# Optimization experiments

Measured on AMD Instinct MI355X. Metric: run time of the kernel, lower is better.

Reference implementation:

```python
import jax, jax.numpy as jnp
import numpy as np
import math

B, S, D = 1, 2048, 2048
H, HD, KV = 16, 128, 1
E, F, TOPK = 8, 4096, 2
EPS = 1e-5


def setup_inputs() -> dict:
    key = jax.random.key(0)
    ks = jax.random.split(key, 14)
    sc = 0.02
    inp = {
        "x": jax.random.normal(ks[0], (B, S, D), dtype=jnp.float32),
        "wq": jax.random.normal(ks[1], (D, H * HD), dtype=jnp.float32) * sc,
        "wk": jax.random.normal(ks[2], (D, KV * HD), dtype=jnp.float32) * sc,
        "wv": jax.random.normal(ks[3], (D, KV * HD), dtype=jnp.float32) * sc,
        "wo": jax.random.normal(ks[4], (H * HD, D), dtype=jnp.float32) * sc,
        "w_router": jax.random.normal(ks[5], (D, E), dtype=jnp.float32) * sc,
        "w1": jax.random.normal(ks[6], (E, D, F), dtype=jnp.float32) * sc,
        "w3": jax.random.normal(ks[7], (E, D, F), dtype=jnp.float32) * sc,
        "w2": jax.random.normal(ks[8], (E, F, D), dtype=jnp.float32) * sc,
        "s_pre_mqa": jnp.ones((D,), dtype=jnp.float32),
        "s_post_mqa": jnp.ones((D,), dtype=jnp.float32),
        "s_pre_moe": jnp.ones((D,), dtype=jnp.float32),
        "s_post_moe": jnp.ones((D,), dtype=jnp.float32),
    }
    return inp


def _rmsnorm(x, scale):
    ms = jnp.mean(x * x, axis=-1, keepdims=True)
    return x * jax.lax.rsqrt(ms + EPS) * scale


def _mqa(h, wq, wk, wv, wo):
    b, s, _ = h.shape
    q = (h @ wq).reshape(b, s, H, HD)
    k = (h @ wk).reshape(b, s, KV, HD)
    v = (h @ wv).reshape(b, s, KV, HD)
    # repeat_interleave kv heads up to H (MQA)
    k = jnp.repeat(k, H // KV, axis=2)
    v = jnp.repeat(v, H // KV, axis=2)
    scale = 1.0 / math.sqrt(HD)
    scores = jnp.einsum("bqhd,bkhd->bhqk", q, k) * scale  # [B,H,S,S]
    causal = jnp.tril(jnp.ones((s, s), dtype=bool))
    scores = jnp.where(causal, scores, jnp.float32(-jnp.inf))
    attn = jax.nn.softmax(scores, axis=-1)
    out = jnp.einsum("bhqk,bkhd->bqhd", attn, v).reshape(b, s, H * HD)
    return out @ wo


def _moe(h, w_router, w1, w2, w3):
    logits = h @ w_router                        # [B,S,E]
    probs = jax.nn.softmax(logits, axis=-1)
    topv, topi = jax.lax.top_k(probs, TOPK)      # [B,S,K]
    topv = topv / jnp.sum(topv, axis=-1, keepdims=True)
    # combine weights per expert: [B,S,E]
    combine = jnp.sum(jax.nn.one_hot(topi, E, dtype=h.dtype) * topv[..., None], axis=-2)
    out = jnp.zeros_like(h)
    for e in range(E):  # fixed small expert count
        ye = (jax.nn.silu(h @ w1[e]) * (h @ w3[e])) @ w2[e]
        out = out + combine[..., e:e + 1] * ye
    return out, combine


def reference(x, wq, wk, wv, wo, w_router, w1, w2, w3,
              s_pre_mqa, s_post_mqa, s_pre_moe, s_post_moe):
    mqa_out = _mqa(_rmsnorm(x, s_pre_mqa), wq, wk, wv, wo)
    x = x + _rmsnorm(mqa_out, s_post_mqa)  # dropout p=0 (eval)
    moe_out, router_mask = _moe(_rmsnorm(x, s_pre_moe), w_router, w1, w2, w3)
    x = x + _rmsnorm(moe_out, s_post_moe)
    return x, router_mask
```

## Files before the change

kernel.cpp:

```cpp
#include <hip/hip_runtime.h>

#define S_LEN 2048
#define DM 2048
#define NHEAD 16
#define HDIM 128
#define NEXP 8
#define FF 4096
#define EPSV 1e-5f

typedef unsigned short u16;
typedef short bf16x8 __attribute__((ext_vector_type(8)));
typedef float f32x4 __attribute__((ext_vector_type(4)));

__device__ __forceinline__ f32x4 mfma16(bf16x8 a, bf16x8 b, f32x4 c) {
  return __builtin_amdgcn_mfma_f32_16x16x32_bf16(a, b, c, 0, 0, 0);
}

__device__ __forceinline__ float bf2f(u16 u) {
  union { unsigned int i; float f; } v; v.i = ((unsigned int)u) << 16; return v.f;
}
__device__ __forceinline__ u16 f2bf(float f) {
  union { float f; unsigned int i; } v; v.f = f;
  unsigned int u = v.i;
  return (u16)((u + 0x7fffu + ((u >> 16) & 1u)) >> 16);
}

__device__ __forceinline__ void gload_lds16(const u16* g, u16* l) {
  __builtin_amdgcn_global_load_lds(
      (const __attribute__((address_space(1))) unsigned int*)(unsigned long long)g,
      (__attribute__((address_space(3))) unsigned int*)(unsigned long long)l, 16, 0, 0);
}

__device__ __forceinline__ float blocksum(float v, float* sh) {
#pragma unroll
  for (int off = 32; off; off >>= 1) v += __shfl_xor(v, off, 64);
  const int w = threadIdx.x >> 6;
  if ((threadIdx.x & 63) == 0) sh[w] = v;
  __syncthreads();
  v = sh[0] + sh[1] + sh[2] + sh[3];
  __syncthreads();
  return v;
}

__device__ __forceinline__ void convsplit_body(char* lds, const float* __restrict__ src,
                                               int ld, u16* __restrict__ dhi,
                                               u16* __restrict__ dlo, int nblk, int kblk) {
  float(*tile)[65] = reinterpret_cast<float(*)[65]>(lds);
  const int n0 = nblk * 64, k0 = kblk * 64;
  const int t = threadIdx.x;
  {
    int r = t >> 4, c4 = (t & 15) * 4;
#pragma unroll
    for (int i = 0; i < 4; ++i) {
      float4 v = *reinterpret_cast<const float4*>(src + (size_t)(k0 + r + i * 16) * ld + n0 + c4);
      tile[r + i * 16][c4 + 0] = v.x;
      tile[r + i * 16][c4 + 1] = v.y;
      tile[r + i * 16][c4 + 2] = v.z;
      tile[r + i * 16][c4 + 3] = v.w;
    }
  }
  __syncthreads();
#pragma unroll
  for (int i = 0; i < 2; ++i) {
    int idx = i * 256 + t;
    int n = idx >> 3, kc = (idx & 7) * 8;
    bf16x8 hi, lo;
#pragma unroll
    for (int j = 0; j < 8; ++j) {
      float f = tile[kc + j][n];
      u16 hv = f2bf(f);
      hi[j] = (short)hv;
      lo[j] = (short)f2bf(f - bf2f(hv));
    }
    size_t o = (size_t)(n0 + n) * 2048 + k0 + kc;
    *reinterpret_cast<bf16x8*>(dhi + o) = hi;
    *reinterpret_cast<bf16x8*>(dlo + o) = lo;
  }
}

__global__ __launch_bounds__(256) void convsplit_kernel(
    const float* __restrict__ src, int ld, u16* __restrict__ dhi, u16* __restrict__ dlo) {
  __shared__ alignas(16) char lds[16640];
  convsplit_body(lds, src, ld, dhi, dlo, blockIdx.x, blockIdx.y);
}

__device__ __forceinline__ void convT_body(char* lds, const float* __restrict__ src,
                                           int R, int C, u16* __restrict__ dst,
                                           int nblk, int rblk, int e) {
  float(*tile)[65] = reinterpret_cast<float(*)[65]>(lds);
  const int n0 = nblk * 64, r0 = rblk * 64;
  const size_t bofs = (size_t)e * R * C;
  const int t = threadIdx.x;
  {
    int r = t >> 4, c4 = (t & 15) * 4;
#pragma unroll
    for (int i = 0; i < 4; ++i) {
      float4 v = *reinterpret_cast<const float4*>(src + bofs + (size_t)(r0 + r + i * 16) * C + n0 + c4);
      tile[r + i * 16][c4 + 0] = v.x;
      tile[r + i * 16][c4 + 1] = v.y;
      tile[r + i * 16][c4 + 2] = v.z;
      tile[r + i * 16][c4 + 3] = v.w;
    }
  }
  __syncthreads();
#pragma unroll
  for (int i = 0; i < 2; ++i) {
    int idx = i * 256 + t;
    int n = idx >> 3, kc = (idx & 7) * 8;
    bf16x8 pk;
#pragma unroll
    for (int j = 0; j < 8; ++j) pk[j] = (short)f2bf(tile[kc + j][n]);
    *reinterpret_cast<bf16x8*>(dst + bofs + (size_t)(n0 + n) * R + r0 + kc) = pk;
  }
}

__global__ __launch_bounds__(256) void rms_pre_kernel(
    const float* __restrict__ x, const float* __restrict__ s, u16* __restrict__ h1) {
  __shared__ float sh[4];
  const int row = blockIdx.x, t = threadIdx.x;
  const float* xr = x + (size_t)row * DM + t * 8;
  float4 a = *reinterpret_cast<const float4*>(xr);
  float4 b = *reinterpret_cast<const float4*>(xr + 4);
  float v[8] = {a.x, a.y, a.z, a.w, b.x, b.y, b.z, b.w};
  float ss = 0.f;
#pragma unroll
  for (int j = 0; j < 8; ++j) ss += v[j] * v[j];
  float inv = rsqrtf(blocksum(ss, sh) * (1.f / DM) + EPSV);
  const float* sp = s + t * 8;
  bf16x8 hi, lo;
#pragma unroll
  for (int j = 0; j < 8; ++j) {
    float val = v[j] * inv * sp[j];
    u16 hv = f2bf(val);
    hi[j] = (short)hv;
    lo[j] = (short)f2bf(val - bf2f(hv));
  }
  *reinterpret_cast<bf16x8*>(h1 + (size_t)row * 4096 + t * 8) = hi;
  *reinterpret_cast<bf16x8*>(h1 + (size_t)row * 4096 + 2048 + t * 8) = lo;
}

__device__ __forceinline__ void gemm3_body(
    char* lds, const u16* __restrict__ A, const u16* __restrict__ Bthi,
    const u16* __restrict__ Btlo, void* __restrict__ out,
    int mblk, int nblk, int mode, int ldc, int lo_off) {
  const int m0 = mblk * 128, n0 = nblk * 64;
  const int t = threadIdx.x, lane = t & 63, w = t >> 6;
  const int wm = (w >> 1) * 64, wn = (w & 1) * 32;
  const int l15 = lane & 15, lg = lane >> 4;
  const int wbase = t & ~63;

  u16* Ah = (u16*)lds;
  u16* Al = (u16*)(lds + 16384);
  u16* Bh = (u16*)(lds + 32768);
  u16* Bl = (u16*)(lds + 40960);

  const u16* Abh = A + (size_t)m0 * 4096;
  const u16* Abl = Abh + 2048;
  const u16* Bbh = Bthi + (size_t)n0 * 2048;
  const u16* Bbl = Btlo + (size_t)n0 * 2048;

  f32x4 acc[4][2];
#pragma unroll
  for (int m = 0; m < 4; ++m)
#pragma unroll
    for (int n = 0; n < 2; ++n) acc[m][n] = (f32x4){0.f, 0.f, 0.f, 0.f};

  for (int k0 = 0; k0 < 2048; k0 += 64) {
    __syncthreads();
#pragma unroll
    for (int i = 0; i < 4; ++i) {
      int p = i * 256 + t;
      int row = p >> 3;
      int csrc = (p & 7) ^ (row & 7);
      gload_lds16(Abh + (size_t)row * 4096 + k0 + csrc * 8, Ah + (i * 256 + wbase) * 8);
      gload_lds16(Abl + (size_t)row * 4096 + k0 + csrc * 8, Al + (i * 256 + wbase) * 8);
    }
#pragma unroll
    for (int i = 0; i < 2; ++i) {
      int p = i * 256 + t;
      int row = p >> 3;
      int csrc = (p & 7) ^ (row & 7);
      gload_lds16(Bbh + (size_t)row * 2048 + k0 + csrc * 8, Bh + (i * 256 + wbase) * 8);
      gload_lds16(Bbl + (size_t)row * 2048 + k0 + csrc * 8, Bl + (i * 256 + wbase) * 8);
    }
    __syncthreads();
#pragma unroll
    for (int kk = 0; kk < 2; ++kk) {
      bf16x8 ah[4], al[4], bh[2], bl[2];
#pragma unroll
      for (int m = 0; m < 4; ++m) {
        int row = wm + m * 16 + l15;
        int byte = row * 128 + (((kk * 4 + lg) * 16) ^ ((row & 7) << 4));
        ah[m] = *reinterpret_cast<const bf16x8*>((const char*)Ah + byte);
        al[m] = *reinterpret_cast<const bf16x8*>((const char*)Al + byte);
      }
#pragma unroll
      for (int n = 0; n < 2; ++n) {
        int row = wn + n * 16 + l15;
        int byte = row * 128 + (((kk * 4 + lg) * 16) ^ ((row & 7) << 4));
        bh[n] = *reinterpret_cast<const bf16x8*>((const char*)Bh + byte);
        bl[n] = *reinterpret_cast<const bf16x8*>((const char*)Bl + byte);
      }
#pragma unroll
      for (int m = 0; m < 4; ++m)
#pragma unroll
        for (int n = 0; n < 2; ++n) {
          acc[m][n] = mfma16(ah[m], bh[n], acc[m][n]);
          acc[m][n] = mfma16(al[m], bh[n], acc[m][n]);
          acc[m][n] = mfma16(ah[m], bl[n], acc[m][n]);
        }
    }
  }
#pragma unroll
  for (int m = 0; m < 4; ++m)
#pragma unroll
    for (int n = 0; n < 2; ++n)
#pragma unroll
      for (int r = 0; r < 4; ++r) {
        int row = m0 + wm + m * 16 + lg * 4 + r;
        int col = n0 + wn + n * 16 + l15;
        float v = acc[m][n][r];
        if (mode == 1) {
          u16* C = (u16*)out;
          u16 hv = f2bf(v);
          C[(size_t)row * ldc + col] = hv;
          C[(size_t)row * ldc + lo_off + col] = f2bf(v - bf2f(hv));
        } else {
          ((float*)out)[(size_t)row * ldc + col] = v;
        }
      }
}

__global__ __launch_bounds__(256) void fat_qkv_conv(
    const u16* __restrict__ A, const u16* __restrict__ Bthi, const u16* __restrict__ Btlo,
    u16* __restrict__ QKV, const float* __restrict__ w1, u16* __restrict__ w1t,
    const float* __restrict__ wo, u16* __restrict__ BtoHi, u16* __restrict__ BtoLo) {
  __shared__ alignas(16) char lds[49152];
  int bid = blockIdx.x;
  if (bid < 576) {
    gemm3_body(lds, A, Bthi, Btlo, QKV, bid % 16, bid / 16, 1, 4608, 2304);
  } else {
    int cid = bid - 576;
    if (cid < 16384)
      convT_body(lds, w1, 2048, 4096, w1t, cid % 64, (cid / 64) % 32, cid / 2048);
    else {
      cid -= 16384;
      convsplit_body(lds, wo, 2048, BtoHi, BtoLo, cid & 31, cid >> 5);
    }
  }
}

__global__ __launch_bounds__(256) void vtrans_kernel(const u16* __restrict__ QKV,
                                                     u16* __restrict__ vt) {
  __shared__ u16 tile[64][65];
  const int s0 = blockIdx.x * 64, c0 = blockIdx.y * 64;
  const int t = threadIdx.x;
#pragma unroll
  for (int i = 0; i < 16; ++i) {
    int idx = i * 256 + t;
    int r = idx >> 6, c = idx & 63;
    int col = c0 + c;
    int src = (col < 128) ? (2176 + col) : (4480 + col - 128);
    tile[r][c] = QKV[(size_t)(s0 + r) * 4608 + src];
  }
  __syncthreads();
#pragma unroll
  for (int i = 0; i < 16; ++i) {
    int idx = i * 256 + t;
    int cc = idx >> 6, ss = idx & 63;
    vt[(size_t)(c0 + cc) * S_LEN + s0 + ss] = tile[ss][cc];
  }
}

__device__ __forceinline__ void attn_body(char* lds, const u16* __restrict__ QKV,
                                          const u16* __restrict__ vt, u16* __restrict__ Os,
                                          int bx, int h) {
  const int qb = 31 - bx;
  const int t = threadIdx.x, w = t >> 6, lane = t & 63;
  const int l15 = lane & 15, lg = lane >> 4;
  const int qr0 = qb * 64 + w * 16;
  const int qrow = qr0 + l15;

  u16* Ks = (u16*)lds;
  u16* Vs = (u16*)(lds + 17408);
  u16* myP = (u16*)(lds + 37888) + w * (16 * 72);

  bf16x8 qf[2][4];
#pragma unroll
  for (int p = 0; p < 2; ++p)
#pragma unroll
    for (int c = 0; c < 4; ++c)
      qf[p][c] = *reinterpret_cast<const bf16x8*>(QKV + (size_t)qrow * 4608 + p * 2304 +
                                                  h * 128 + c * 32 + lg * 8);

  f32x4 o[8];
#pragma unroll
  for (int n = 0; n < 8; ++n) o[n] = (f32x4){0.f, 0.f, 0.f, 0.f};
  f32x4 lracc = (f32x4){0.f, 0.f, 0.f, 0.f};
  bf16x8 onesf;
#pragma unroll
  for (int j = 0; j < 8; ++j) onesf[j] = (short)0x3F80;

  const float scale = 0.08838834764831845f;
  const int kend = qb * 64 + 64;

  for (int j0 = 0; j0 < kend; j0 += 32) {
    __syncthreads();
#pragma unroll
    for (int i = 0; i < 4; ++i) {
      int idx = i * 256 + t;
      int row = idx >> 5, seg = idx & 31;
      int srccol = (seg < 16) ? (2048 + seg * 8) : (4352 + (seg - 16) * 8);
      bf16x8 v = *reinterpret_cast<const bf16x8*>(QKV + (size_t)(j0 + row) * 4608 + srccol);
      *reinterpret_cast<bf16x8*>(&Ks[row * 272 + seg * 8]) = v;
    }
#pragma unroll
    for (int i = 0; i < 4; ++i) {
      int idx = i * 256 + t;
      int row = idx >> 2, seg = idx & 3;
      bf16x8 v = *reinterpret_cast<const bf16x8*>(vt + (size_t)row * S_LEN + j0 + seg * 8);
      *reinterpret_cast<bf16x8*>(&Vs[row * 40 + seg * 8]) = v;
    }
    __syncthreads();

    if (j0 > qr0 + 15) continue;
    f32x4 sc[2];
#pragma unroll
    for (int half = 0; half < 2; ++half) {
      const int kb = (half * 16 + l15) * 272;
      f32x4 a0 = (f32x4){0.f, 0.f, 0.f, 0.f};
      f32x4 a1 = (f32x4){0.f, 0.f, 0.f, 0.f};
      f32x4 a2 = (f32x4){0.f, 0.f, 0.f, 0.f};
#pragma unroll
      for (int cc = 0; cc < 4; ++cc) {
        bf16x8 kh = *reinterpret_cast<const bf16x8*>(&Ks[kb + cc * 32 + lg * 8]);
        a0 = mfma16(qf[0][cc], kh, a0);
        a1 = mfma16(qf[1][cc], kh, a1);
      }
#pragma unroll
      for (int cc = 0; cc < 4; ++cc) {
        bf16x8 kl = *reinterpret_cast<const bf16x8*>(&Ks[kb + 128 + cc * 32 + lg * 8]);
        a2 = mfma16(qf[0][cc], kl, a2);
      }
      f32x4 a = (a0 + a1) + a2;
#pragma unroll
      for (int r = 0; r < 4; ++r) {
        int rowg = qr0 + lg * 4 + r;
        int colg = j0 + half * 16 + l15;
        sc[half][r] = (colg <= rowg) ? a[r] * scale : -1e30f;
      }
    }
#pragma unroll
    for (int r = 0; r < 4; ++r) {
      float p0 = __expf(sc[0][r]);
      float p1 = __expf(sc[1][r]);
      int lrow = lg * 4 + r;
      u16 h0 = f2bf(p0), h1v = f2bf(p1);
      myP[lrow * 72 + l15] = h0;
      myP[lrow * 72 + 16 + l15] = h1v;
      myP[lrow * 72 + 32 + l15] = f2bf(p0 - bf2f(h0));
      myP[lrow * 72 + 48 + l15] = f2bf(p1 - bf2f(h1v));
    }
    bf16x8 pfh = *reinterpret_cast<const bf16x8*>(myP + l15 * 72 + lg * 8);
    bf16x8 pfl = *reinterpret_cast<const bf16x8*>(myP + l15 * 72 + 32 + lg * 8);

    lracc = mfma16(pfh, onesf, lracc);
    lracc = mfma16(pfl, onesf, lracc);

#pragma unroll
    for (int n = 0; n < 8; ++n) {
      bf16x8 vh = *reinterpret_cast<const bf16x8*>(&Vs[(n * 16 + l15) * 40 + lg * 8]);
      bf16x8 vl = *reinterpret_cast<const bf16x8*>(&Vs[(n * 16 + l15 + 128) * 40 + lg * 8]);
      o[n] = mfma16(pfh, vh, o[n]);
      o[n] = mfma16(pfl, vh, o[n]);
      o[n] = mfma16(pfh, vl, o[n]);
    }
  }
#pragma unroll
  for (int n = 0; n < 8; ++n)
#pragma unroll
    for (int r = 0; r < 4; ++r) {
      int rowg = qr0 + lg * 4 + r;
      float v = o[n][r] / lracc[r];
      u16 hv = f2bf(v);
      Os[(size_t)rowg * 4096 + h * 128 + n * 16 + l15] = hv;
      Os[(size_t)rowg * 4096 + 2048 + h * 128 + n * 16 + l15] = f2bf(v - bf2f(hv));
    }
}

__global__ __launch_bounds__(256) void fat_attn_conv(
    const u16* __restrict__ QKV, const u16* __restrict__ vt, u16* __restrict__ Os,
    const float* __restrict__ w3, u16* __restrict__ w3t) {
  __shared__ alignas(16) char lds[47104];
  int bid = blockIdx.x;
  if (bid < 512) {
    attn_body(lds, QKV, vt, Os, bid & 31, bid >> 5);
  } else {
    int cid = bid - 512;
    convT_body(lds, w3, 2048, 4096, w3t, cid % 64, (cid / 64) % 32, cid / 2048);
  }
}

__global__ __launch_bounds__(256) void fat_wo_conv(
    const u16* __restrict__ A, const u16* __restrict__ Bthi, const u16* __restrict__ Btlo,
    float* __restrict__ out, const float* __restrict__ w2, u16* __restrict__ w2t) {
  __shared__ alignas(16) char lds[49152];
  int bid = blockIdx.x;
  if (bid < 512) {
    gemm3_body(lds, A, Bthi, Btlo, out, bid & 15, bid >> 4, 2, 2048, 0);
  } else {
    int cid = bid - 512;
    convT_body(lds, w2, 4096, 2048, w2t, cid % 32, (cid / 32) % 64, cid / 2048);
  }
}

__global__ __launch_bounds__(256) void rms_mid_router(
    const float* __restrict__ x, const float* __restrict__ mqa,
    const float* __restrict__ spost, const float* __restrict__ spre,
    const float* __restrict__ wr, float* __restrict__ x1, u16* __restrict__ h2b,
    float* __restrict__ comb, int* __restrict__ topi, float* __restrict__ topw,
    int* __restrict__ cnt) {
  __shared__ float sh1[4];
  __shared__ float sh2[4];
  __shared__ float red[4][8];
  __shared__ float lgits[8];
  const int row = blockIdx.x, t = threadIdx.x;
  const size_t base = (size_t)row * DM + t * 8;
  float mv[8];
  {
    float4 a0 = *reinterpret_cast<const float4*>(mqa + base);
    float4 b0 = *reinterpret_cast<const float4*>(mqa + base + 4);
    mv[0] = a0.x; mv[1] = a0.y; mv[2] = a0.z; mv[3] = a0.w;
    mv[4] = b0.x; mv[5] = b0.y; mv[6] = b0.z; mv[7] = b0.w;
  }
  float ss1 = 0.f;
#pragma unroll
  for (int j = 0; j < 8; ++j) ss1 += mv[j] * mv[j];
  float inv1 = rsqrtf(blocksum(ss1, sh1) * (1.f / DM) + EPSV);
  float4 xa = *reinterpret_cast<const float4*>(x + base);
  float4 xb = *reinterpret_cast<const float4*>(x + base + 4);
  float xv[8] = {xa.x, xa.y, xa.z, xa.w, xb.x, xb.y, xb.z, xb.w};
  float x1v[8];
  float ss2 = 0.f;
#pragma unroll
  for (int j = 0; j < 8; ++j) {
    x1v[j] = xv[j] + mv[j] * inv1 * spost[t * 8 + j];
    ss2 += x1v[j] * x1v[j];
  }
  float inv2 = rsqrtf(blocksum(ss2, sh2) * (1.f / DM) + EPSV);
  *reinterpret_cast<float4*>(x1 + base) = make_float4(x1v[0], x1v[1], x1v[2], x1v[3]);
  *reinterpret_cast<float4*>(x1 + base + 4) = make_float4(x1v[4], x1v[5], x1v[6], x1v[7]);
  float hv[8];
  bf16x8 hb;
#pragma unroll
  for (int j = 0; j < 8; ++j) {
    hv[j] = x1v[j] * inv2 * spre[t * 8 + j];
    hb[j] = (short)f2bf(hv[j]);
  }
  *reinterpret_cast<bf16x8*>(h2b + base) = hb;

  float acc[8] = {0.f, 0.f, 0.f, 0.f, 0.f, 0.f, 0.f, 0.f};
  const float* wrow = wr + (size_t)t * 64;
#pragma unroll
  for (int j = 0; j < 8; ++j) {
    const float* wj = wrow + j * 8;
#pragma unroll
    for (int e = 0; e < 8; ++e) acc[e] += hv[j] * wj[e];
  }
#pragma unroll
  for (int off = 32; off; off >>= 1)
#pragma unroll
    for (int e = 0; e < 8; ++e) acc[e] += __shfl_xor(acc[e], off, 64);
  const int w = t >> 6;
  if ((t & 63) == 0) {
#pragma unroll
    for (int e = 0; e < 8; ++e) red[w][e] = acc[e];
  }
  __syncthreads();
  if (t < 8) lgits[t] = red[0][t] + red[1][t] + red[2][t] + red[3][t];
  __syncthreads();
  if (t == 0) {
    float L[8], mx = -1e30f;
#pragma unroll
    for (int e = 0; e < 8; ++e) {
      L[e] = lgits[e];
      mx = fmaxf(mx, L[e]);
    }
    float p[8], s = 0.f;
#pragma unroll
    for (int e = 0; e < 8; ++e) {
      p[e] = expf(L[e] - mx);
      s += p[e];
    }
#pragma unroll
    for (int e = 0; e < 8; ++e) p[e] /= s;
    int e0 = 0;
    for (int e = 1; e < 8; ++e)
      if (p[e] > p[e0]) e0 = e;
    int e1 = (e0 == 0) ? 1 : 0;
    for (int e = 0; e < 8; ++e)
      if (e != e0 && p[e] > p[e1]) e1 = e;
    float ssum = p[e0] + p[e1];
    float w0 = p[e0] / ssum, w1 = p[e1] / ssum;
    for (int e = 0; e < 8; ++e)
      comb[(size_t)row * 8 + e] = (e == e0) ? w0 : ((e == e1) ? w1 : 0.f);
    topi[2 * row] = e0;
    topi[2 * row + 1] = e1;
    topw[2 * row] = w0;
    topw[2 * row + 1] = w1;
    atomicAdd(&cnt[e0], 1);
    atomicAdd(&cnt[e1], 1);
  }
}

__global__ void zero_meta_kernel(int* __restrict__ cnt) {
  if (threadIdx.x < NEXP) cnt[threadIdx.x] = 0;
}

__global__ void build_meta_kernel(const int* __restrict__ cnt, int* __restrict__ cursor,
                                  int* __restrict__ meta) {
  if (threadIdx.x != 0) return;
  int off = 0, nt = 0;
  for (int e = 0; e < NEXP; ++e) {
    int c = cnt[e];
    cursor[e] = off;
    int ntl = (c + 255) >> 8;
    for (int r = 0; r < ntl; ++r) {
      meta[8 + nt] = e;
      meta[64 + nt] = off + r * 256;
      int rem = c - r * 256;
      meta[120 + nt] = rem < 256 ? rem : 256;
      ++nt;
    }
    off += c;
  }
  meta[0] = nt;
}

__global__ void scatter_kernel(const int* __restrict__ topi, int* __restrict__ cursor,
                               int* __restrict__ ptok, int* __restrict__ pos_of) {
  int token = blockIdx.x * 256 + threadIdx.x;
  if (token >= S_LEN) return;
  for (int k = 0; k < 2; ++k) {
    int e = topi[2 * token + k];
    int pos = atomicAdd(&cursor[e], 1);
    ptok[pos] = token;
    pos_of[2 * token + k] = pos;
  }
}

__global__ __launch_bounds__(512) void moe_gemm1b(
    const u16* __restrict__ H2, const u16* __restrict__ W1t, const u16* __restrict__ W3t,
    u16* __restrict__ U, const int* __restrict__ meta, const int* __restrict__ ptok) {
  const int tile = blockIdx.x;
  if (tile >= meta[0]) return;
  const int e = meta[8 + tile], row0 = meta[64 + tile], rows = meta[120 + tile];
  const int n0 = blockIdx.y * 64;
  const u16* B1 = W1t + (size_t)e * FF * DM + (size_t)n0 * 2048;
  const u16* B3 = W3t + (size_t)e * FF * DM + (size_t)n0 * 2048;
  const int t = threadIdx.x, lane = t & 63, w = t >> 6;
  const int wm = (w >> 1) * 64, wn = (w & 1) * 32;
  const int l15 = lane & 15, lg = lane >> 4;
  const int wbase = t & ~63;

  __shared__ alignas(16) u16 As[16384];
  __shared__ alignas(16) u16 B1s[4096];
  __shared__ alignas(16) u16 B3s[4096];
  __shared__ int toks[256];
  if (t < 256) toks[t] = (t < rows) ? ptok[row0 + t] : ptok[row0];
  __syncthreads();

  f32x4 aG[4][2], aT[4][2];
#pragma unroll
  for (int m = 0; m < 4; ++m)
#pragma unroll
    for (int n = 0; n < 2; ++n) {
      aG[m][n] = (f32x4){0.f, 0.f, 0.f, 0.f};
      aT[m][n] = (f32x4){0.f, 0.f, 0.f, 0.f};
    }

  for (int k0 = 0; k0 < DM; k0 += 64) {
    __syncthreads();
#pragma unroll
    for (int i = 0; i < 4; ++i) {
      int p = i * 512 + t;
      int row = p >> 3;
      int csrc = (p & 7) ^ (row & 7);
      gload_lds16(H2 + (size_t)toks[row] * DM + k0 + csrc * 8, As + (i * 512 + wbase) * 8);
    }
    {
      int row = t >> 3;
      int csrc = (t & 7) ^ (row & 7);
      gload_lds16(B1 + (size_t)row * 2048 + k0 + csrc * 8, B1s + wbase * 8);
      gload_lds16(B3 + (size_t)row * 2048 + k0 + csrc * 8, B3s + wbase * 8);
    }
    __syncthreads();
#pragma unroll
    for (int kk = 0; kk < 2; ++kk) {
      bf16x8 af[4], b1f[2], b3f[2];
#pragma unroll
      for (int m = 0; m < 4; ++m) {
        int row = wm + m * 16 + l15;
        int byte = row * 128 + (((kk * 4 + lg) * 16) ^ ((row & 7) << 4));
        af[m] = *reinterpret_cast<const bf16x8*>((const char*)As + byte);
      }
#pragma unroll
      for (int n = 0; n < 2; ++n) {
        int row = wn + n * 16 + l15;
        int byte = row * 128 + (((kk * 4 + lg) * 16) ^ ((row & 7) << 4));
        b1f[n] = *reinterpret_cast<const bf16x8*>((const char*)B1s + byte);
        b3f[n] = *reinterpret_cast<const bf16x8*>((const char*)B3s + byte);
      }
#pragma unroll
      for (int m = 0; m < 4; ++m)
#pragma unroll
        for (int n = 0; n < 2; ++n) {
          aG[m][n] = mfma16(af[m], b1f[n], aG[m][n]);
          aT[m][n] = mfma16(af[m], b3f[n], aT[m][n]);
        }
    }
  }
#pragma unroll
  for (int m = 0; m < 4; ++m)
#pragma unroll
    for (int n = 0; n < 2; ++n)
#pragma unroll
      for (int r = 0; r < 4; ++r) {
        int lrow = wm + m * 16 + lg * 4 + r;
        if (lrow < rows) {
          float g = aG[m][n][r], tt = aT[m][n][r];
          float u = (g / (1.f + __expf(-g))) * tt;
          U[(size_t)(row0 + lrow) * FF + n0 + wn + n * 16 + l15] = f2bf(u);
        }
      }
}

__global__ __launch_bounds__(512) void moe_gemm2b(
    const u16* __restrict__ U, const u16* __restrict__ W2t, u16* __restrict__ Y,
    const int* __restrict__ meta) {
  const int tile = blockIdx.x;
  if (tile >= meta[0]) return;
  const int e = meta[8 + tile], row0 = meta[64 + tile], rows = meta[120 + tile];
  const int n0 = blockIdx.y * 128;
  const u16* Bb = W2t + (size_t)e * DM * FF + (size_t)n0 * 4096;
  const int t = threadIdx.x, lane = t & 63, w = t >> 6;
  const int wm = (w >> 1) * 64, wn = (w & 1) * 64;
  const int l15 = lane & 15, lg = lane >> 4;
  const int wbase = t & ~63;

  __shared__ alignas(16) u16 As[16384];
  __shared__ alignas(16) u16 Bs[8192];

  f32x4 acc[4][4];
#pragma unroll
  for (int m = 0; m < 4; ++m)
#pragma unroll
    for (int n = 0; n < 4; ++n) acc[m][n] = (f32x4){0.f, 0.f, 0.f, 0.f};

  for (int k0 = 0; k0 < FF; k0 += 64) {
    __syncthreads();
#pragma unroll
    for (int i = 0; i < 4; ++i) {
      int p = i * 512 + t;
      int row = p >> 3;
      int csrc = (p & 7) ^ (row & 7);
      gload_lds16(U + (size_t)(row0 + row) * FF + k0 + csrc * 8, As + (i * 512 + wbase) * 8);
    }
#pragma unroll
    for (int i = 0; i < 2; ++i) {
      int p = i * 512 + t;
      int row = p >> 3;
      int csrc = (p & 7) ^ (row & 7);
      gload_lds16(Bb + (size_t)row * 4096 + k0 + csrc * 8, Bs + (i * 512 + wbase) * 8);
    }
    __syncthreads();
#pragma unroll
    for (int kk = 0; kk < 2; ++kk) {
      bf16x8 af[4], bfr[4];
#pragma unroll
      for (int m = 0; m < 4; ++m) {
        int row = wm + m * 16 + l15;
        int byte = row * 128 + (((kk * 4 + lg) * 16) ^ ((row & 7) << 4));
        af[m] = *reinterpret_cast<const bf16x8*>((const char*)As + byte);
      }
#pragma unroll
      for (int n = 0; n < 4; ++n) {
        int row = wn + n * 16 + l15;
        int byte = row * 128 + (((kk * 4 + lg) * 16) ^ ((row & 7) << 4));
        bfr[n] = *reinterpret_cast<const bf16x8*>((const char*)Bs + byte);
      }
#pragma unroll
      for (int m = 0; m < 4; ++m)
#pragma unroll
        for (int n = 0; n < 4; ++n) acc[m][n] = mfma16(af[m], bfr[n], acc[m][n]);
    }
  }
#pragma unroll
  for (int m = 0; m < 4; ++m)
#pragma unroll
    for (int n = 0; n < 4; ++n)
#pragma unroll
      for (int r = 0; r < 4; ++r) {
        int lrow = wm + m * 16 + lg * 4 + r;
        if (lrow < rows)
          Y[(size_t)(row0 + lrow) * DM + n0 + wn + n * 16 + l15] = f2bf(acc[m][n][r]);
      }
}

__global__ __launch_bounds__(256) void moe_final_kernel(
    const float* __restrict__ x1, const u16* __restrict__ Y,
    const int* __restrict__ pos_of, const float* __restrict__ topw,
    const float* __restrict__ spost, float* __restrict__ xout) {
  __shared__ float sh[4];
  const int row = blockIdx.x, t = threadIdx.x;
  const int p0 = pos_of[2 * row], p1 = pos_of[2 * row + 1];
  const float w0 = topw[2 * row], w1 = topw[2 * row + 1];
  bf16x8 y0 = *reinterpret_cast<const bf16x8*>(Y + (size_t)p0 * DM + t * 8);
  bf16x8 y1 = *reinterpret_cast<const bf16x8*>(Y + (size_t)p1 * DM + t * 8);
  float mv[8];
  float ss = 0.f;
#pragma unroll
  for (int j = 0; j < 8; ++j) {
    mv[j] = w0 * bf2f((u16)y0[j]) + w1 * bf2f((u16)y1[j]);
    ss += mv[j] * mv[j];
  }
  float inv = rsqrtf(blocksum(ss, sh) * (1.f / DM) + EPSV);
  const size_t base = (size_t)row * DM + t * 8;
#pragma unroll
  for (int j = 0; j < 8; ++j)
    xout[base + j] = x1[base + j] + mv[j] * inv * spost[t * 8 + j];
}

extern "C" void kernel_launch(void* const* d_in, const int* in_sizes, int n_in,
                              void* d_out, int out_size, void* d_ws, size_t ws_size,
                              hipStream_t stream) {
  (void)in_sizes; (void)n_in; (void)out_size; (void)ws_size;
  const float* x = (const float*)d_in[0];
  const float* wq = (const float*)d_in[1];
  const float* wk = (const float*)d_in[2];
  const float* wv = (const float*)d_in[3];
  const float* wo = (const float*)d_in[4];
  const float* wrt = (const float*)d_in[5];
  const float* w1 = (const float*)d_in[6];
  const float* w3 = (const float*)d_in[7];
  const float* w2 = (const float*)d_in[8];
  const float* s_pre_mqa = (const float*)d_in[9];
  const float* s_post_mqa = (const float*)d_in[10];
  const float* s_pre_moe = (const float*)d_in[11];
  const float* s_post_moe = (const float*)d_in[12];

  float* xout = (float*)d_out;
  float* out_router = xout + (size_t)S_LEN * DM;

  char* wsp = (char*)d_ws;
  size_t off = 0;
  auto alloc = [&](size_t n) {
    char* p = wsp + off;
    off += (n + 255) & ~(size_t)255;
    return p;
  };
  u16* U = (u16*)alloc((size_t)4096 * FF * 2);
  u16* Y = (u16*)alloc((size_t)4096 * DM * 2);
  float* mqa = (float*)alloc((size_t)S_LEN * DM * 4);
  u16* h1s = (u16*)alloc((size_t)S_LEN * 4096 * 2);
  u16* attn_s = h1s;
  u16* Btq_hi = (u16*)alloc((size_t)2304 * 2048 * 2);
  u16* Btq_lo = (u16*)alloc((size_t)2304 * 2048 * 2);
  u16* Bto_hi = (u16*)alloc((size_t)2048 * 2048 * 2);
  u16* Bto_lo = (u16*)alloc((size_t)2048 * 2048 * 2);
  u16* QKV = (u16*)alloc((size_t)S_LEN * 4608 * 2);
  u16* vt = (u16*)alloc((size_t)256 * S_LEN * 2);
  float* x1 = (float*)alloc((size_t)S_LEN * DM * 4);
  u16* h2b = (u16*)alloc((size_t)S_LEN * DM * 2);
  int* topi = (int*)alloc(4096 * 4);
  float* topw = (float*)alloc(4096 * 4);
  int* pos_of = (int*)alloc(4096 * 4);
  int* ptok = (int*)alloc(4352 * 4);
  int* cnt = (int*)alloc(32 * 4);
  int* cursor = (int*)alloc(32 * 4);
  int* meta = (int*)alloc(256 * 4);
  u16* w1t = (u16*)alloc((size_t)NEXP * DM * FF * 2);
  u16* w3t = (u16*)alloc((size_t)NEXP * DM * FF * 2);
  u16* w2t = (u16*)alloc((size_t)NEXP * FF * DM * 2);

  dim3 B256(256);
  dim3 B512(512);

  convsplit_kernel<<<dim3(32, 32), B256, 0, stream>>>(wq, 2048, Btq_hi, Btq_lo);
  convsplit_kernel<<<dim3(2, 32), B256, 0, stream>>>(wk, 128, Btq_hi + (size_t)2048 * 2048,
                                                     Btq_lo + (size_t)2048 * 2048);
  convsplit_kernel<<<dim3(2, 32), B256, 0, stream>>>(wv, 128, Btq_hi + (size_t)2176 * 2048,
                                                     Btq_lo + (size_t)2176 * 2048);

  rms_pre_kernel<<<dim3(S_LEN), B256, 0, stream>>>(x, s_pre_mqa, h1s);
  fat_qkv_conv<<<dim3(576 + 16384 + 1024), B256, 0, stream>>>(
      h1s, Btq_hi, Btq_lo, QKV, w1, w1t, wo, Bto_hi, Bto_lo);
  vtrans_kernel<<<dim3(32, 4), B256, 0, stream>>>(QKV, vt);
  fat_attn_conv<<<dim3(512 + 16384), B256, 0, stream>>>(QKV, vt, attn_s, w3, w3t);
  fat_wo_conv<<<dim3(512 + 16384), B256, 0, stream>>>(attn_s, Bto_hi, Bto_lo, mqa, w2, w2t);
  zero_meta_kernel<<<dim3(1), dim3(64), 0, stream>>>(cnt);
  rms_mid_router<<<dim3(S_LEN), B256, 0, stream>>>(x, mqa, s_post_mqa, s_pre_moe, wrt,
                                                   x1, h2b, out_router, topi, topw, cnt);
  build_meta_kernel<<<dim3(1), dim3(64), 0, stream>>>(cnt, cursor, meta);
  scatter_kernel<<<dim3(8), B256, 0, stream>>>(topi, cursor, ptok, pos_of);
  moe_gemm1b<<<dim3(24, 64), B512, 0, stream>>>(h2b, w1t, w3t, U, meta, ptok);
  moe_gemm2b<<<dim3(24, 16), B512, 0, stream>>>(U, w2t, Y, meta);
  moe_final_kernel<<<dim3(S_LEN), B256, 0, stream>>>(x1, Y, pos_of, topw, s_post_moe, xout);
}
```

Baseline: 824.0 us.

## Fuse pre-norm with QKV weight conversion and overlap w2 transpose with MoE gemm1

Merges rms_pre and the three wq/wk/wv split-conversion launches into one fat kernel. Moves the w2 transpose-conversion out of the wo GEMM launch and into the MoE gemm1 launch using a new 512-thread transpose body, leaving wo GEMM as a standalone kernel. The aim is fewer launches and better overlap of weight conversion with compute. Risk: conversion blocks now compete with the MoE gemm1 tiles, and the early-return path in gemm1 blocks is fine since meta is checked per block.

Result: no change. 817.4 us (-0.8%).

```diff
diff --git a/kernel.cpp b/kernel.cpp
--- a/kernel.cpp
+++ b/kernel.cpp
@@ -76,12 +76,6 @@
     *reinterpret_cast<bf16x8*>(dhi + o) = hi;
     *reinterpret_cast<bf16x8*>(dlo + o) = lo;
   }
-}
-
-__global__ __launch_bounds__(256) void convsplit_kernel(
-    const float* __restrict__ src, int ld, u16* __restrict__ dhi, u16* __restrict__ dlo) {
-  __shared__ alignas(16) char lds[16640];
-  convsplit_body(lds, src, ld, dhi, dlo, blockIdx.x, blockIdx.y);
 }
 
 __device__ __forceinline__ void convT_body(char* lds, const float* __restrict__ src,
@@ -114,10 +108,38 @@
   }
 }
 
-__global__ __launch_bounds__(256) void rms_pre_kernel(
-    const float* __restrict__ x, const float* __restrict__ s, u16* __restrict__ h1) {
-  __shared__ float sh[4];
-  const int row = blockIdx.x, t = threadIdx.x;
+__device__ __forceinline__ void convT_body512(char* lds, const float* __restrict__ src,
+                                              int R, int C, u16* __restrict__ dst,
+                                              int nblk, int rblk, int e) {
+  float(*tile)[65] = reinterpret_cast<float(*)[65]>(lds);
+  const int n0 = nblk * 64, r0 = rblk * 64;
+  const size_t bofs = (size_t)e * R * C;
+  const int t = threadIdx.x;
+#pragma unroll
+  for (int i = 0; i < 2; ++i) {
+    int p = i * 512 + t;
+    int r = p >> 4, c4 = (p & 15) * 4;
+    float4 v = *reinterpret_cast<const float4*>(src + bofs + (size_t)(r0 + r) * C + n0 + c4);
+    tile[r][c4 + 0] = v.x;
+    tile[r][c4 + 1] = v.y;
+    tile[r][c4 + 2] = v.z;
+    tile[r][c4 + 3] = v.w;
+  }
+  __syncthreads();
+  {
+    int n = t >> 3, kc = (t & 7) * 8;
+    bf16x8 pk;
+#pragma unroll
+    for (int j = 0; j < 8; ++j) pk[j] = (short)f2bf(tile[kc + j][n]);
+    *reinterpret_cast<bf16x8*>(dst + bofs + (size_t)(n0 + n) * R + r0 + kc) = pk;
+  }
+}
+
+__device__ __forceinline__ void rms_pre_body(char* lds, const float* __restrict__ x,
+                                             const float* __restrict__ s,
+                                             u16* __restrict__ h1, int row) {
+  float* sh = (float*)lds;
+  const int t = threadIdx.x;
   const float* xr = x + (size_t)row * DM + t * 8;
   float4 a = *reinterpret_cast<const float4*>(xr);
   float4 b = *reinterpret_cast<const float4*>(xr + 4);
@@ -137,6 +159,28 @@
   }
   *reinterpret_cast<bf16x8*>(h1 + (size_t)row * 4096 + t * 8) = hi;
   *reinterpret_cast<bf16x8*>(h1 + (size_t)row * 4096 + 2048 + t * 8) = lo;
+}
+
+__global__ __launch_bounds__(256) void fat_pre(
+    const float* __restrict__ x, const float* __restrict__ spre, u16* __restrict__ h1,
+    const float* __restrict__ wq, const float* __restrict__ wk, const float* __restrict__ wv,
+    u16* __restrict__ BtqHi, u16* __restrict__ BtqLo) {
+  __shared__ alignas(16) char lds[16640];
+  int bid = blockIdx.x;
+  if (bid < 2048) {
+    rms_pre_body(lds, x, spre, h1, bid);
+  } else if (bid < 3072) {
+    int c = bid - 2048;
+    convsplit_body(lds, wq, 2048, BtqHi, BtqLo, c & 31, c >> 5);
+  } else if (bid < 3136) {
+    int c = bid - 3072;
+    convsplit_body(lds, wk, 128, BtqHi + (size_t)2048 * 2048, BtqLo + (size_t)2048 * 2048,
+                   c & 1, c >> 1);
+  } else {
+    int c = bid - 3136;
+    convsplit_body(lds, wv, 128, BtqHi + (size_t)2176 * 2048, BtqLo + (size_t)2176 * 2048,
+                   c & 1, c >> 1);
+  }
 }
 
 __device__ __forceinline__ void gemm3_body(
@@ -229,6 +273,13 @@
           ((float*)out)[(size_t)row * ldc + col] = v;
         }
       }
+}
+
+__global__ __launch_bounds__(256) void gemm3_kernel(
+    const u16* __restrict__ A, const u16* __restrict__ Bthi, const u16* __restrict__ Btlo,
+    float* __restrict__ out) {
+  __shared__ alignas(16) char lds[49152];
+  gemm3_body(lds, A, Bthi, Btlo, out, blockIdx.x, blockIdx.y, 2, 2048, 0);
 }
 
 __global__ __launch_bounds__(256) void fat_qkv_conv(
@@ -398,19 +449,6 @@
   } else {
     int cid = bid - 512;
     convT_body(lds, w3, 2048, 4096, w3t, cid % 64, (cid / 64) % 32, cid / 2048);
-  }
-}
-
-__global__ __launch_bounds__(256) void fat_wo_conv(
-    const u16* __restrict__ A, const u16* __restrict__ Bthi, const u16* __restrict__ Btlo,
-    float* __restrict__ out, const float* __restrict__ w2, u16* __restrict__ w2t) {
-  __shared__ alignas(16) char lds[49152];
-  int bid = blockIdx.x;
-  if (bid < 512) {
-    gemm3_body(lds, A, Bthi, Btlo, out, bid & 15, bid >> 4, 2, 2048, 0);
-  } else {
-    int cid = bid - 512;
-    convT_body(lds, w2, 4096, 2048, w2t, cid % 32, (cid / 32) % 64, cid / 2048);
   }
 }
 
@@ -549,13 +587,14 @@
   }
 }
 
-__global__ __launch_bounds__(512) void moe_gemm1b(
+__device__ __forceinline__ void moe_gemm1_body(
+    u16* As, u16* B1s, u16* B3s, int* toks,
     const u16* __restrict__ H2, const u16* __restrict__ W1t, const u16* __restrict__ W3t,
-    u16* __restrict__ U, const int* __restrict__ meta, const int* __restrict__ ptok) {
-  const int tile = blockIdx.x;
+    u16* __restrict__ U, const int* __restrict__ meta, const int* __restrict__ ptok,
+    int tile, int n0blk) {
   if (tile >= meta[0]) return;
   const int e = meta[8 + tile], row0 = meta[64 + tile], rows = meta[120 + tile];
-  const int n0 = blockIdx.y * 64;
+  const int n0 = n0blk * 64;
   const u16* B1 = W1t + (size_t)e * FF * DM + (size_t)n0 * 2048;
   const u16* B3 = W3t + (size_t)e * FF * DM + (size_t)n0 * 2048;
   const int t = threadIdx.x, lane = t & 63, w = t >> 6;
@@ -563,10 +602,6 @@
   const int l15 = lane & 15, lg = lane >> 4;
   const int wbase = t & ~63;
 
-  __shared__ alignas(16) u16 As[16384];
-  __shared__ alignas(16) u16 B1s[4096];
-  __shared__ alignas(16) u16 B3s[4096];
-  __shared__ int toks[256];
   if (t < 256) toks[t] = (t < rows) ? ptok[row0 + t] : ptok[row0];
   __syncthreads();
 
@@ -633,6 +668,23 @@
           U[(size_t)(row0 + lrow) * FF + n0 + wn + n * 16 + l15] = f2bf(u);
         }
       }
+}
+
+__global__ __launch_bounds__(512) void fat_moe1(
+    const u16* __restrict__ H2, const u16* __restrict__ W1t, const u16* __restrict__ W3t,
+    u16* __restrict__ U, const int* __restrict__ meta, const int* __restrict__ ptok,
+    const float* __restrict__ w2, u16* __restrict__ w2t) {
+  __shared__ alignas(16) u16 As[16384];
+  __shared__ alignas(16) u16 B1s[4096];
+  __shared__ alignas(16) u16 B3s[4096];
+  __shared__ int toks[256];
+  int bid = blockIdx.x;
+  if (bid < 1536) {
+    moe_gemm1_body(As, B1s, B3s, toks, H2, W1t, W3t, U, meta, ptok, bid % 24, bid / 24);
+  } else {
+    int cid = bid - 1536;
+    convT_body512((char*)As, w2, 4096, 2048, w2t, cid % 32, (cid / 32) % 64, cid / 2048);
+  }
 }
 
 __global__ __launch_bounds__(512) void moe_gemm2b(
@@ -786,24 +838,18 @@
   dim3 B256(256);
   dim3 B512(512);
 
-  convsplit_kernel<<<dim3(32, 32), B256, 0, stream>>>(wq, 2048, Btq_hi, Btq_lo);
-  convsplit_kernel<<<dim3(2, 32), B256, 0, stream>>>(wk, 128, Btq_hi + (size_t)2048 * 2048,
-                                                     Btq_lo + (size_t)2048 * 2048);
-  convsplit_kernel<<<dim3(2, 32), B256, 0, stream>>>(wv, 128, Btq_hi + (size_t)2176 * 2048,
-                                                     Btq_lo + (size_t)2176 * 2048);
-
-  rms_pre_kernel<<<dim3(S_LEN), B256, 0, stream>>>(x, s_pre_mqa, h1s);
+  fat_pre<<<dim3(3200), B256, 0, stream>>>(x, s_pre_mqa, h1s, wq, wk, wv, Btq_hi, Btq_lo);
   fat_qkv_conv<<<dim3(576 + 16384 + 1024), B256, 0, stream>>>(
       h1s, Btq_hi, Btq_lo, QKV, w1, w1t, wo, Bto_hi, Bto_lo);
   vtrans_kernel<<<dim3(32, 4), B256, 0, stream>>>(QKV, vt);
   fat_attn_conv<<<dim3(512 + 16384), B256, 0, stream>>>(QKV, vt, attn_s, w3, w3t);
-  fat_wo_conv<<<dim3(512 + 16384), B256, 0, stream>>>(attn_s, Bto_hi, Bto_lo, mqa, w2, w2t);
+  gemm3_kernel<<<dim3(16, 32), B256, 0, stream>>>(attn_s, Bto_hi, Bto_lo, mqa);
   zero_meta_kernel<<<dim3(1), dim3(64), 0, stream>>>(cnt);
   rms_mid_router<<<dim3(S_LEN), B256, 0, stream>>>(x, mqa, s_post_mqa, s_pre_moe, wrt,
                                                    x1, h2b, out_router, topi, topw, cnt);
   build_meta_kernel<<<dim3(1), dim3(64), 0, stream>>>(cnt, cursor, meta);
   scatter_kernel<<<dim3(8), B256, 0, stream>>>(topi, cursor, ptok, pos_of);
-  moe_gemm1b<<<dim3(24, 64), B512, 0, stream>>>(h2b, w1t, w3t, U, meta, ptok);
+  fat_moe1<<<dim3(1536 + 16384), B512, 0, stream>>>(h2b, w1t, w3t, U, meta, ptok, w2, w2t);
   moe_gemm2b<<<dim3(24, 16), B512, 0, stream>>>(U, w2t, Y, meta);
   moe_final_kernel<<<dim3(S_LEN), B256, 0, stream>>>(x1, Y, pos_of, topw, s_post_moe, xout);
 }
```
